# Kernel tuning notes

Measured on AMD Instinct MI355X. Metric: run time of the kernel, lower is better.

Reference implementation:

```python
import jax, jax.numpy as jnp
import numpy as np

B, S, D, H = 2, 2048, 1024, 16
DK = D // H


def setup_inputs() -> dict:
    key = jax.random.key(0)
    ks = jax.random.split(key, 8)
    xavier = lambda k, shape: jax.random.uniform(k, shape, jnp.float32, -1.0, 1.0) * np.sqrt(6.0 / (shape[0] + shape[1]))
    return {
        "query": jax.random.normal(ks[0], (B, S, D), jnp.float32),
        "key": jax.random.normal(ks[1], (B, S, D), jnp.float32),
        "value": jax.random.normal(ks[2], (B, S, D), jnp.float32),
        # causal mask: True above the diagonal -> masked out
        "mask": jnp.broadcast_to(jnp.triu(jnp.ones((S, S), bool), k=1), (B, S, S)),
        "w_q": xavier(ks[3], (D, D)),  # torch Linear weight [out, in]
        "w_k": xavier(ks[4], (D, D)),
        "w_v": xavier(ks[5], (D, D)),
        "w_o": xavier(ks[6], (D, D)),
        "b_o": jnp.zeros((D,), jnp.float32),
    }


def reference(query, key, value, mask, w_q, w_k, w_v, w_o, b_o):
    b, sq, d = query.shape
    sk = key.shape[1]
    # projections (torch Linear: x @ W.T)
    Q = (query @ w_q.T).reshape(b, sq, H, DK).transpose(0, 2, 1, 3)  # [B,H,Sq,DK]
    K = (key @ w_k.T).reshape(b, sk, H, DK).transpose(0, 2, 1, 3)
    V = (value @ w_v.T).reshape(b, sk, H, DK).transpose(0, 2, 1, 3)
    scores = jnp.einsum('bhqd,bhkd->bhqk', Q, K) / np.sqrt(DK)
    scores = jnp.where(mask[:, None, :, :], jnp.float32(-1e9), scores)
    attn = jax.nn.softmax(scores, axis=-1)  # dropout is identity in eval
    out = jnp.einsum('bhqk,bhkd->bhqd', attn, V)
    out = out.transpose(0, 2, 1, 3).reshape(b, sq, d)
    return out @ w_o.T + b_o
```

## Files before the change

kernel.cpp:

```cpp
#include <hip/hip_runtime.h>
#include <hip/hip_bf16.h>
#include <stdint.h>


typedef __attribute__((ext_vector_type(4))) float  f32x4;
typedef __attribute__((ext_vector_type(4))) int    i32x4;
typedef __attribute__((ext_vector_type(8))) __bf16 bf16x8;
typedef __attribute__((ext_vector_type(4))) __bf16 bf16x4;
typedef __attribute__((ext_vector_type(2))) __bf16 bf16x2;

#define MFMA16(a, b, c) __builtin_amdgcn_mfma_f32_16x16x32_bf16((a), (b), (c), 0, 0, 0)

__device__ __forceinline__ void async16(const void* g, void* lds) {
  __builtin_amdgcn_global_load_lds(
      (const __attribute__((address_space(1))) uint32_t*)g,
      (__attribute__((address_space(3))) uint32_t*)lds,
      16, 0, 0);
}

__device__ __forceinline__ bf16x8 lds_swz_read(const __bf16* base, int row, int cchunk) {
  const int sw = cchunk ^ (row & 7);
  return *(const bf16x8*)((const char*)base + row * 128 + sw * 16);
}

__global__ void detect_dtype(const uint16_t* __restrict__ w, int* __restrict__ flag) {
  __shared__ int s;
  if (threadIdx.x == 0) s = 0;
  __syncthreads();
  int big = 0;
  for (int i = threadIdx.x; i < 8192; i += 256) {
    uint32_t u = ((uint32_t)w[i]) << 16;
    float f;
    __builtin_memcpy(&f, &u, 4);
    if (fabsf(f) > 1.0f) big = 1;
  }
  if (big) atomicOr(&s, 1);
  __syncthreads();
  if (threadIdx.x == 0) *flag = s;
}

struct CvtArgs { const void* src[8]; void* dst[8]; int n[8]; };

__global__ __launch_bounds__(256)
void convert_all(CvtArgs a, const int* __restrict__ flagp) {
  if (*flagp == 0) return;
  const int t = blockIdx.y;
  const int n = a.n[t];
  const int i0 = (blockIdx.x * 256 + threadIdx.x) * 8;
  if (i0 >= n) return;
  const float* s = (const float*)a.src[t];
  __bf16* d = (__bf16*)a.dst[t];
  bf16x8 v;
#pragma unroll
  for (int j = 0; j < 8; ++j) v[j] = (__bf16)s[i0 + j];
  *(bf16x8*)(d + i0) = v;
}

struct GemmArgs {
  const __bf16* A[3];    const __bf16* W[3];
  const __bf16* Acvt[3]; const __bf16* Wcvt[3];
  void* C[3]; float scale[3];
  const __bf16* bias; const __bf16* biascvt;
  const int* flagp; int mode;
};

__global__ __launch_bounds__(256, 3)
void gemm_nt(GemmArgs ga)
{
  constexpr int K = 1024;
  __shared__ __align__(16) __bf16 smem[8704];
  __bf16* As = smem;
  __bf16* Bs = smem + 4096;

  const int id = blockIdx.x + (blockIdx.y << 3) + (blockIdx.z << 8);
  const int mb = (id & 7) * 4 + ((id >> 3) & 3);
  const int rest = id >> 5;
  const int nb = rest & 7;
  const int z = rest >> 3;

  const int f = *ga.flagp;
  const __bf16* __restrict__ A = f ? ga.Acvt[z] : ga.A[z];
  const __bf16* __restrict__ W = f ? ga.Wcvt[z] : ga.W[z];
  void* __restrict__ C = ga.C[z];
  const float scale = ga.scale[z];
  const int mode = ga.mode;

  const int tid = threadIdx.x;
  const int lane = tid & 63;
  const int wave = tid >> 6;
  const int l15 = lane & 15;
  const int quad = lane >> 4;
  const int bm = mb * 128;
  const int bn = nb * 128;
  const int wm = (wave >> 1) * 64;
  const int wn = (wave & 1) * 64;

  f32x4 acc[4][4];
#pragma unroll
  for (int mi = 0; mi < 4; ++mi)
#pragma unroll
    for (int ni = 0; ni < 4; ++ni) {
      f32x4 zz = {0.f, 0.f, 0.f, 0.f};
      acc[mi][ni] = zz;
    }

  for (int kt = 0; kt < K / 32; ++kt) {
    const int k0 = kt * 32;
    __syncthreads();
#pragma unroll
    for (int r = 0; r < 2; ++r) {
      const int chunk = r * 256 + wave * 64 + lane;
      const int row = chunk >> 2, c = chunk & 3;
      async16(A + (size_t)(bm + row) * K + k0 + c * 8, As + (r * 256 + wave * 64) * 8);
      async16(W + (size_t)(bn + row) * K + k0 + c * 8, Bs + (r * 256 + wave * 64) * 8);
    }
    __syncthreads();

    bf16x8 af[4];
    bf16x8 bfr[4];
#pragma unroll
    for (int mi = 0; mi < 4; ++mi)
      af[mi] = *(const bf16x8*)(As + (wm + mi * 16 + l15) * 32 + quad * 8);
#pragma unroll
    for (int ni = 0; ni < 4; ++ni)
      bfr[ni] = *(const bf16x8*)(Bs + (wn + ni * 16 + l15) * 32 + quad * 8);
#pragma unroll
    for (int mi = 0; mi < 4; ++mi)
#pragma unroll
      for (int ni = 0; ni < 4; ++ni)
        acc[mi][ni] = MFMA16(af[mi], bfr[ni], acc[mi][ni]);
  }

  float bv[4] = {0.f, 0.f, 0.f, 0.f};
  if (mode == 1) {
    const __bf16* bias = f ? ga.biascvt : ga.bias;
#pragma unroll
    for (int ni = 0; ni < 4; ++ni) bv[ni] = (float)bias[bn + wn + ni * 16 + l15];
  }
  __bf16 (*Cs)[136] = (__bf16(*)[136])smem;

#pragma unroll
  for (int pass = 0; pass < 2; ++pass) {
    __syncthreads();
    if ((wave >> 1) == pass) {
#pragma unroll
      for (int mi = 0; mi < 4; ++mi)
#pragma unroll
        for (int ni = 0; ni < 4; ++ni)
#pragma unroll
          for (int r = 0; r < 4; ++r)
            Cs[mi * 16 + quad * 4 + r][wn + ni * 16 + l15] =
                (__bf16)(acc[mi][ni][r] * scale + bv[ni]);
    }
    __syncthreads();

    if (mode == 0) {
#pragma unroll
      for (int it = 0; it < 4; ++it) {
        const int cid = it * 256 + tid;
        const int off = cid & 7, seg = cid >> 3;
        const int hl = seg & 1, rowl = seg >> 1;
        f32x4 v = *(const f32x4*)(&Cs[rowl][hl * 64 + off * 8]);
        const int m = bm + pass * 64 + rowl;
        const int b = m >> 11, s = m & 2047;
        const int h = (bn >> 6) + hl;
        *(f32x4*)((__bf16*)C + ((size_t)(b * 16 + h) * 2048 + s) * 64 + off * 8) = v;
      }
    } else if (f) {
#pragma unroll
      for (int it = 0; it < 4; ++it) {
        const int cid = it * 256 + tid;
        const int off = cid & 15, rowl = cid >> 4;
        bf16x8 vb = *(const bf16x8*)(&Cs[rowl][off * 8]);
        const int m = bm + pass * 64 + rowl;
        float* dst = (float*)C + (size_t)m * 1024 + bn + off * 8;
        f32x4 lo, hi;
#pragma unroll
        for (int j = 0; j < 4; ++j) { lo[j] = (float)vb[j]; hi[j] = (float)vb[4 + j]; }
        *(f32x4*)dst = lo;
        *(f32x4*)(dst + 4) = hi;
      }
    } else {
#pragma unroll
      for (int it = 0; it < 4; ++it) {
        const int cid = it * 256 + tid;
        const int off = cid & 15, rowl = cid >> 4;
        bf16x8 vb = *(const bf16x8*)(&Cs[rowl][off * 8]);
        const int m = bm + pass * 64 + rowl;
        *(bf16x8*)((__bf16*)C + (size_t)m * 1024 + bn + off * 8) = vb;
      }
    }
  }
}

__global__ __launch_bounds__(256, 3)
void attn(const __bf16* __restrict__ Q,
          const __bf16* __restrict__ Kg,
          const __bf16* __restrict__ Vg,
          __bf16* __restrict__ O)
{
  __shared__ __align__(16) __bf16 Ks[2][128 * 64];
  __shared__ __align__(16) __bf16 Vts[64][136];

  const int tid = threadIdx.x;
  const int lane = tid & 63;
  const int wave = tid >> 6;
  const int l15 = lane & 15;
  const int quad = lane >> 4;

  const int zb = blockIdx.x;
  const int qt = 31 - (zb >> 5);
  const int bh = zb & 31;
  const int q0 = qt * 64;
  const int nIter = (qt >> 1) + 1;

  const __bf16* Qp = Q + (size_t)bh * 2048 * 64;
  const __bf16* Kp = Kg + (size_t)bh * 2048 * 64;
  const __bf16* Vp = Vg + (size_t)bh * 2048 * 64;

  const int qrow_wl = wave * 16 + l15;

  bf16x8 qf[2];
#pragma unroll
  for (int kc = 0; kc < 2; ++kc)
    qf[kc] = *(const bf16x8*)(Qp + (size_t)(q0 + qrow_wl) * 64 + kc * 32 + quad * 8);

  f32x4 o_[4];
#pragma unroll
  for (int dt = 0; dt < 4; ++dt) {
    f32x4 zz = {0.f, 0.f, 0.f, 0.f};
    o_[dt] = zz;
  }
  float lsum = 0.0f;

  const int pp4 = tid & 31;
  const int dgg = tid >> 5;
  const int P0 = (((pp4 & 0x18) | ((pp4 & 3) << 1) | ((pp4 >> 2) & 1)) << 2);

#pragma unroll
  for (int r = 0; r < 4; ++r) {
    const int chunk = r * 256 + tid;
    const int row = chunk >> 3, c = (chunk & 7) ^ (row & 7);
    async16(Kp + (size_t)row * 64 + c * 8,
            (char*)&Ks[0][0] + (r * 256 + wave * 64) * 16);
  }
  bf16x8 va0 = *(const bf16x8*)(Vp + (size_t)(4 * pp4 + 0) * 64 + dgg * 8);
  bf16x8 va1 = *(const bf16x8*)(Vp + (size_t)(4 * pp4 + 1) * 64 + dgg * 8);
  bf16x8 va2 = *(const bf16x8*)(Vp + (size_t)(4 * pp4 + 2) * 64 + dgg * 8);
  bf16x8 va3 = *(const bf16x8*)(Vp + (size_t)(4 * pp4 + 3) * 64 + dgg * 8);

  for (int t = 0; t < nIter; ++t) {
    const int cur = t & 1;

#pragma unroll
    for (int j = 0; j < 8; ++j) {
      bf16x4 w = { va0[j], va1[j], va2[j], va3[j] };
      *(bf16x4*)(&Vts[dgg * 8 + j][P0]) = w;
    }
    __syncthreads();

    bf16x8 vn0 = va0, vn1 = va1, vn2 = va2, vn3 = va3;
    if (t + 1 < nIter) {
      const int k1 = (t + 1) * 128;
#pragma unroll
      for (int r = 0; r < 4; ++r) {
        const int chunk = r * 256 + tid;
        const int row = chunk >> 3, c = (chunk & 7) ^ (row & 7);
        async16(Kp + (size_t)(k1 + row) * 64 + c * 8,
                (char*)&Ks[cur ^ 1][0] + (r * 256 + wave * 64) * 16);
      }
      vn0 = *(const bf16x8*)(Vp + (size_t)(k1 + 4 * pp4 + 0) * 64 + dgg * 8);
      vn1 = *(const bf16x8*)(Vp + (size_t)(k1 + 4 * pp4 + 1) * 64 + dgg * 8);
      vn2 = *(const bf16x8*)(Vp + (size_t)(k1 + 4 * pp4 + 2) * 64 + dgg * 8);
      vn3 = *(const bf16x8*)(Vp + (size_t)(k1 + 4 * pp4 + 3) * 64 + dgg * 8);
    }

    f32x4 st[8];
#pragma unroll
    for (int nt = 0; nt < 8; ++nt) {
      f32x4 zz = {0.f, 0.f, 0.f, 0.f};
      st[nt] = zz;
    }
    __builtin_amdgcn_s_setprio(1);
#pragma unroll
    for (int kc = 0; kc < 2; ++kc)
#pragma unroll
      for (int nt = 0; nt < 8; ++nt) {
        bf16x8 kf = lds_swz_read(&Ks[cur][0], nt * 16 + l15, kc * 4 + quad);
        st[nt] = MFMA16(kf, qf[kc], st[nt]);
      }
    __builtin_amdgcn_s_setprio(0);

    if (t == (qt >> 1)) {
      const int k0 = t * 128;
#pragma unroll
      for (int nt = 0; nt < 8; ++nt)
#pragma unroll
        for (int r = 0; r < 4; ++r)
          if (k0 + nt * 16 + quad * 4 + r > q0 + qrow_wl) st[nt][r] = -1e30f;
    }

    bf16x8 pf[4];
#pragma unroll
    for (int nt = 0; nt < 8; ++nt)
#pragma unroll
      for (int r = 0; r < 4; ++r) {
        const float pv = __builtin_amdgcn_exp2f(st[nt][r]);
        lsum += pv;
        pf[nt >> 1][(nt & 1) * 4 + r] = (__bf16)pv;
      }

    __builtin_amdgcn_s_setprio(1);
#pragma unroll
    for (int kc = 0; kc < 4; ++kc)
#pragma unroll
      for (int dt = 0; dt < 4; ++dt) {
        bf16x8 vf = *(const bf16x8*)(&Vts[dt * 16 + l15][kc * 32 + quad * 8]);
        o_[dt] = MFMA16(vf, pf[kc], o_[dt]);
      }
    __builtin_amdgcn_s_setprio(0);

    __syncthreads();
    va0 = vn0; va1 = vn1; va2 = vn2; va3 = vn3;
  }

  lsum += __shfl_xor(lsum, 16, 64);
  lsum += __shfl_xor(lsum, 32, 64);

  __bf16 (*Ot)[72] = (__bf16(*)[72])&Vts[0][0];
  const float inv_l = 1.0f / lsum;
#pragma unroll
  for (int dt = 0; dt < 4; ++dt)
#pragma unroll
    for (int r = 0; r < 4; r += 2) {
      bf16x2 pr = { (__bf16)(o_[dt][r] * inv_l),
                    (__bf16)(o_[dt][r + 1] * inv_l) };
      *(bf16x2*)(&Ot[qrow_wl][dt * 16 + quad * 4 + r]) = pr;
    }
  __syncthreads();

  const int b = bh >> 4, h = bh & 15;
#pragma unroll
  for (int t = 0; t < 2; ++t) {
    const int i = t * 256 + tid;
    const int row = i >> 3, c = i & 7;
    f32x4 v = *(const f32x4*)(&Ot[row][c * 8]);
    *(f32x4*)(O + (size_t)(b * 2048 + q0 + row) * 1024 + h * 64 + c * 8) = v;
  }
}

extern "C" void kernel_launch(void* const* d_in, const int* in_sizes, int n_in,
                              void* d_out, int out_size, void* d_ws, size_t ws_size,
                              hipStream_t stream) {
  char* ws = (char*)d_ws;
  int* flag = (int*)ws;
  __bf16* Xc0 = (__bf16*)(ws + (1u << 20));
  __bf16* Xc1 = (__bf16*)(ws + (9u << 20));
  __bf16* Xc2 = (__bf16*)(ws + (17u << 20));
  __bf16* Wc0 = (__bf16*)(ws + (25u << 20));
  __bf16* Wc1 = (__bf16*)(ws + (27u << 20));
  __bf16* Wc2 = (__bf16*)(ws + (29u << 20));
  __bf16* Wc3 = (__bf16*)(ws + (31u << 20));
  __bf16* bc  = (__bf16*)(ws + (33u << 20));
  __bf16* Qw  = (__bf16*)(ws + (34u << 20));
  __bf16* Kw  = (__bf16*)(ws + (42u << 20));
  __bf16* Vw  = (__bf16*)(ws + (50u << 20));
  __bf16* Aw  = (__bf16*)(ws + (58u << 20));

  detect_dtype<<<1, 256, 0, stream>>>((const uint16_t*)d_in[4], flag);

  CvtArgs ca;
  ca.src[0] = d_in[0]; ca.dst[0] = Xc0; ca.n[0] = 4194304;
  ca.src[1] = d_in[1]; ca.dst[1] = Xc1; ca.n[1] = 4194304;
  ca.src[2] = d_in[2]; ca.dst[2] = Xc2; ca.n[2] = 4194304;
  ca.src[3] = d_in[4]; ca.dst[3] = Wc0; ca.n[3] = 1048576;
  ca.src[4] = d_in[5]; ca.dst[4] = Wc1; ca.n[4] = 1048576;
  ca.src[5] = d_in[6]; ca.dst[5] = Wc2; ca.n[5] = 1048576;
  ca.src[6] = d_in[7]; ca.dst[6] = Wc3; ca.n[6] = 1048576;
  ca.src[7] = d_in[8]; ca.dst[7] = bc;  ca.n[7] = 1024;
  convert_all<<<dim3(2048, 8), 256, 0, stream>>>(ca, flag);

  GemmArgs g0;
  g0.A[0] = (const __bf16*)d_in[0]; g0.Acvt[0] = Xc0;
  g0.A[1] = (const __bf16*)d_in[1]; g0.Acvt[1] = Xc1;
  g0.A[2] = (const __bf16*)d_in[2]; g0.Acvt[2] = Xc2;
  g0.W[0] = (const __bf16*)d_in[4]; g0.Wcvt[0] = Wc0;
  g0.W[1] = (const __bf16*)d_in[5]; g0.Wcvt[1] = Wc1;
  g0.W[2] = (const __bf16*)d_in[6]; g0.Wcvt[2] = Wc2;
  g0.C[0] = Qw; g0.scale[0] = 0.18033688f;
  g0.C[1] = Kw; g0.scale[1] = 1.0f;
  g0.C[2] = Vw; g0.scale[2] = 1.0f;
  g0.bias = nullptr; g0.biascvt = nullptr; g0.flagp = flag; g0.mode = 0;
  gemm_nt<<<dim3(8, 32, 3), 256, 0, stream>>>(g0);

  attn<<<dim3(1024), 256, 0, stream>>>(Qw, Kw, Vw, Aw);

  GemmArgs g1;
  g1.A[0] = Aw; g1.Acvt[0] = Aw;
  g1.A[1] = nullptr; g1.Acvt[1] = nullptr;
  g1.A[2] = nullptr; g1.Acvt[2] = nullptr;
  g1.W[0] = (const __bf16*)d_in[7]; g1.Wcvt[0] = Wc3;
  g1.W[1] = nullptr; g1.Wcvt[1] = nullptr;
  g1.W[2] = nullptr; g1.Wcvt[2] = nullptr;
  g1.C[0] = d_out; g1.scale[0] = 1.0f;
  g1.C[1] = nullptr; g1.scale[1] = 0.f;
  g1.C[2] = nullptr; g1.scale[2] = 0.f;
  g1.bias = (const __bf16*)d_in[8]; g1.biascvt = bc;
  g1.flagp = flag; g1.mode = 1;
  gemm_nt<<<dim3(8, 32, 1), 256, 0, stream>>>(g1);
}
```

Baseline: 229.8 us.

## Double-buffer GEMM LDS tiles and double attention query tile per block

The GEMM now uses two LDS buffers, prefetching the next K-slice while MFMAs run on the current one, and drops one barrier per iteration. The attention kernel processes 128 query rows per block (two 16-row groups per wave) instead of 64, so each K/V tile loaded into LDS is reused twice, and it launches half as many blocks. This cuts global/LDS traffic per query but raises register pressure (launch bounds lowered to 2 waves) and reduces block-level parallelism and causal load balance.

Result: no change. 234.0 us (+1.9%).

```diff
diff --git a/kernel.cpp b/kernel.cpp
--- a/kernel.cpp
+++ b/kernel.cpp
@@ -68,9 +68,7 @@
 void gemm_nt(GemmArgs ga)
 {
   constexpr int K = 1024;
-  __shared__ __align__(16) __bf16 smem[8704];
-  __bf16* As = smem;
-  __bf16* Bs = smem + 4096;
+  __shared__ __align__(16) __bf16 smem[16384];
 
   const int id = blockIdx.x + (blockIdx.y << 3) + (blockIdx.z << 8);
   const int mb = (id & 7) * 4 + ((id >> 3) & 3);
@@ -95,18 +93,10 @@
   const int wm = (wave >> 1) * 64;
   const int wn = (wave & 1) * 64;
 
-  f32x4 acc[4][4];
-#pragma unroll
-  for (int mi = 0; mi < 4; ++mi)
-#pragma unroll
-    for (int ni = 0; ni < 4; ++ni) {
-      f32x4 zz = {0.f, 0.f, 0.f, 0.f};
-      acc[mi][ni] = zz;
-    }
-
-  for (int kt = 0; kt < K / 32; ++kt) {
+  auto stage = [&](int kt, int buf) {
     const int k0 = kt * 32;
-    __syncthreads();
+    __bf16* As = smem + buf * 8192;
+    __bf16* Bs = As + 4096;
 #pragma unroll
     for (int r = 0; r < 2; ++r) {
       const int chunk = r * 256 + wave * 64 + lane;
@@ -114,8 +104,26 @@
       async16(A + (size_t)(bm + row) * K + k0 + c * 8, As + (r * 256 + wave * 64) * 8);
       async16(W + (size_t)(bn + row) * K + k0 + c * 8, Bs + (r * 256 + wave * 64) * 8);
     }
-    __syncthreads();
-
+  };
+
+  f32x4 acc[4][4];
+#pragma unroll
+  for (int mi = 0; mi < 4; ++mi)
+#pragma unroll
+    for (int ni = 0; ni < 4; ++ni) {
+      f32x4 zz = {0.f, 0.f, 0.f, 0.f};
+      acc[mi][ni] = zz;
+    }
+
+  stage(0, 0);
+  __syncthreads();
+
+  for (int kt = 0; kt < K / 32; ++kt) {
+    const int cur = kt & 1;
+    if (kt + 1 < K / 32) stage(kt + 1, cur ^ 1);
+
+    const __bf16* As = smem + cur * 8192;
+    const __bf16* Bs = As + 4096;
     bf16x8 af[4];
     bf16x8 bfr[4];
 #pragma unroll
@@ -129,6 +137,8 @@
 #pragma unroll
       for (int ni = 0; ni < 4; ++ni)
         acc[mi][ni] = MFMA16(af[mi], bfr[ni], acc[mi][ni]);
+
+    __syncthreads();
   }
 
   float bv[4] = {0.f, 0.f, 0.f, 0.f};
@@ -193,7 +203,7 @@
   }
 }
 
-__global__ __launch_bounds__(256, 3)
+__global__ __launch_bounds__(256, 2)
 void attn(const __bf16* __restrict__ Q,
           const __bf16* __restrict__ Kg,
           const __bf16* __restrict__ Vg,
@@ -209,29 +219,32 @@
   const int quad = lane >> 4;
 
   const int zb = blockIdx.x;
-  const int qt = 31 - (zb >> 5);
+  const int qt = 15 - (zb >> 5);
   const int bh = zb & 31;
-  const int q0 = qt * 64;
-  const int nIter = (qt >> 1) + 1;
+  const int q0 = qt * 128;
+  const int nIter = qt + 1;
 
   const __bf16* Qp = Q + (size_t)bh * 2048 * 64;
   const __bf16* Kp = Kg + (size_t)bh * 2048 * 64;
   const __bf16* Vp = Vg + (size_t)bh * 2048 * 64;
 
-  const int qrow_wl = wave * 16 + l15;
-
-  bf16x8 qf[2];
-#pragma unroll
-  for (int kc = 0; kc < 2; ++kc)
-    qf[kc] = *(const bf16x8*)(Qp + (size_t)(q0 + qrow_wl) * 64 + kc * 32 + quad * 8);
-
-  f32x4 o_[4];
+  const int qrA = wave * 32 + l15;
+  const int qrB = qrA + 16;
+
+  bf16x8 qfA[2], qfB[2];
+#pragma unroll
+  for (int kc = 0; kc < 2; ++kc) {
+    qfA[kc] = *(const bf16x8*)(Qp + (size_t)(q0 + qrA) * 64 + kc * 32 + quad * 8);
+    qfB[kc] = *(const bf16x8*)(Qp + (size_t)(q0 + qrB) * 64 + kc * 32 + quad * 8);
+  }
+
+  f32x4 oA[4], oB[4];
 #pragma unroll
   for (int dt = 0; dt < 4; ++dt) {
     f32x4 zz = {0.f, 0.f, 0.f, 0.f};
-    o_[dt] = zz;
-  }
-  float lsum = 0.0f;
+    oA[dt] = zz; oB[dt] = zz;
+  }
+  float lsA = 0.0f, lsB = 0.0f;
 
   const int pp4 = tid & 31;
   const int dgg = tid >> 5;
@@ -275,11 +288,11 @@
       vn3 = *(const bf16x8*)(Vp + (size_t)(k1 + 4 * pp4 + 3) * 64 + dgg * 8);
     }
 
-    f32x4 st[8];
+    f32x4 stA[8], stB[8];
 #pragma unroll
     for (int nt = 0; nt < 8; ++nt) {
       f32x4 zz = {0.f, 0.f, 0.f, 0.f};
-      st[nt] = zz;
+      stA[nt] = zz; stB[nt] = zz;
     }
     __builtin_amdgcn_s_setprio(1);
 #pragma unroll
@@ -287,27 +300,32 @@
 #pragma unroll
       for (int nt = 0; nt < 8; ++nt) {
         bf16x8 kf = lds_swz_read(&Ks[cur][0], nt * 16 + l15, kc * 4 + quad);
-        st[nt] = MFMA16(kf, qf[kc], st[nt]);
+        stA[nt] = MFMA16(kf, qfA[kc], stA[nt]);
+        stB[nt] = MFMA16(kf, qfB[kc], stB[nt]);
       }
     __builtin_amdgcn_s_setprio(0);
 
-    if (t == (qt >> 1)) {
-      const int k0 = t * 128;
+    if (t == qt) {
 #pragma unroll
       for (int nt = 0; nt < 8; ++nt)
 #pragma unroll
-        for (int r = 0; r < 4; ++r)
-          if (k0 + nt * 16 + quad * 4 + r > q0 + qrow_wl) st[nt][r] = -1e30f;
-    }
-
-    bf16x8 pf[4];
+        for (int r = 0; r < 4; ++r) {
+          const int kk = nt * 16 + quad * 4 + r;
+          if (kk > qrA) stA[nt][r] = -1e30f;
+          if (kk > qrB) stB[nt][r] = -1e30f;
+        }
+    }
+
+    bf16x8 pfA[4], pfB[4];
 #pragma unroll
     for (int nt = 0; nt < 8; ++nt)
 #pragma unroll
       for (int r = 0; r < 4; ++r) {
-        const float pv = __builtin_amdgcn_exp2f(st[nt][r]);
-        lsum += pv;
-        pf[nt >> 1][(nt & 1) * 4 + r] = (__bf16)pv;
+        const float pA = __builtin_amdgcn_exp2f(stA[nt][r]);
+        const float pB = __builtin_amdgcn_exp2f(stB[nt][r]);
+        lsA += pA; lsB += pB;
+        pfA[nt >> 1][(nt & 1) * 4 + r] = (__bf16)pA;
+        pfB[nt >> 1][(nt & 1) * 4 + r] = (__bf16)pB;
       }
 
     __builtin_amdgcn_s_setprio(1);
@@ -316,7 +334,8 @@
 #pragma unroll
       for (int dt = 0; dt < 4; ++dt) {
         bf16x8 vf = *(const bf16x8*)(&Vts[dt * 16 + l15][kc * 32 + quad * 8]);
-        o_[dt] = MFMA16(vf, pf[kc], o_[dt]);
+        oA[dt] = MFMA16(vf, pfA[kc], oA[dt]);
+        oB[dt] = MFMA16(vf, pfB[kc], oB[dt]);
       }
     __builtin_amdgcn_s_setprio(0);
 
@@ -324,24 +343,28 @@
     va0 = vn0; va1 = vn1; va2 = vn2; va3 = vn3;
   }
 
-  lsum += __shfl_xor(lsum, 16, 64);
-  lsum += __shfl_xor(lsum, 32, 64);
-
-  __bf16 (*Ot)[72] = (__bf16(*)[72])&Vts[0][0];
-  const float inv_l = 1.0f / lsum;
+  lsA += __shfl_xor(lsA, 16, 64);
+  lsA += __shfl_xor(lsA, 32, 64);
+  lsB += __shfl_xor(lsB, 16, 64);
+  lsB += __shfl_xor(lsB, 32, 64);
+
+  __bf16 (*Ot)[72] = (__bf16(*)[72])&Ks[0][0];
+  const float invA = 1.0f / lsA;
+  const float invB = 1.0f / lsB;
 #pragma unroll
   for (int dt = 0; dt < 4; ++dt)
 #pragma unroll
     for (int r = 0; r < 4; r += 2) {
-      bf16x2 pr = { (__bf16)(o_[dt][r] * inv_l),
-                    (__bf16)(o_[dt][r + 1] * inv_l) };
-      *(bf16x2*)(&Ot[qrow_wl][dt * 16 + quad * 4 + r]) = pr;
+      bf16x2 pa = { (__bf16)(oA[dt][r] * invA), (__bf16)(oA[dt][r + 1] * invA) };
+      *(bf16x2*)(&Ot[qrA][dt * 16 + quad * 4 + r]) = pa;
+      bf16x2 pb = { (__bf16)(oB[dt][r] * invB), (__bf16)(oB[dt][r + 1] * invB) };
+      *(bf16x2*)(&Ot[qrB][dt * 16 + quad * 4 + r]) = pb;
     }
   __syncthreads();
 
   const int b = bh >> 4, h = bh & 15;
 #pragma unroll
-  for (int t = 0; t < 2; ++t) {
+  for (int t = 0; t < 4; ++t) {
     const int i = t * 256 + tid;
     const int row = i >> 3, c = i & 7;
     f32x4 v = *(const f32x4*)(&Ot[row][c * 8]);
@@ -393,7 +416,7 @@
   g0.bias = nullptr; g0.biascvt = nullptr; g0.flagp = flag; g0.mode = 0;
   gemm_nt<<<dim3(8, 32, 3), 256, 0, stream>>>(g0);
 
-  attn<<<dim3(1024), 256, 0, stream>>>(Qw, Kw, Vw, Aw);
+  attn<<<dim3(512), 256, 0, stream>>>(Qw, Kw, Vw, Aw);
 
   GemmArgs g1;
   g1.A[0] = Aw; g1.Acvt[0] = Aw;
```
